# Performance work log

Measured on AMD Instinct MI355X. Metric: run time of the kernel, lower is better.

## Reference

```python
import jax, jax.numpy as jnp
import numpy as np

INPUT_DIM = 32
HIDDEN = 64
BATCH = 4096
SEQ = 256


def _uniform(key, shape, bound):
    return jax.random.uniform(key, shape, dtype=jnp.float32, minval=-bound, maxval=bound)


def setup_inputs() -> dict:
    key = jax.random.key(0)
    ks = jax.random.split(key, 16)
    kb = 1.0 / np.sqrt(HIDDEN)  # torch LSTM/Linear init bound
    x = jax.random.normal(ks[0], (BATCH, SEQ, INPUT_DIM), dtype=jnp.float32)
    # LSTM layer 0 (input_dim -> hidden), gate order i,f,g,o stacked on dim 0
    Wih0 = _uniform(ks[1], (4 * HIDDEN, INPUT_DIM), kb)
    Whh0 = _uniform(ks[2], (4 * HIDDEN, HIDDEN), kb)
    bih0 = _uniform(ks[3], (4 * HIDDEN,), kb)
    bhh0 = _uniform(ks[4], (4 * HIDDEN,), kb)
    # LSTM layer 1 (hidden -> hidden)
    Wih1 = _uniform(ks[5], (4 * HIDDEN, HIDDEN), kb)
    Whh1 = _uniform(ks[6], (4 * HIDDEN, HIDDEN), kb)
    bih1 = _uniform(ks[7], (4 * HIDDEN,), kb)
    bhh1 = _uniform(ks[8], (4 * HIDDEN,), kb)
    # MLP head
    W1 = _uniform(ks[9], (HIDDEN, HIDDEN), kb)
    b1 = _uniform(ks[10], (HIDDEN,), kb)
    W2 = _uniform(ks[11], (1, HIDDEN), kb)
    b2 = _uniform(ks[12], (1,), kb)
    return {"x": x, "Wih0": Wih0, "Whh0": Whh0, "bih0": bih0, "bhh0": bhh0,
            "Wih1": Wih1, "Whh1": Whh1, "bih1": bih1, "bhh1": bhh1,
            "W1": W1, "b1": b1, "W2": W2, "b2": b2}


def lstm_layer(x, Wih, Whh, bih, bhh):
    """x: [B,T,D] -> hidden sequence [B,T,H]. PyTorch gate order i,f,g,o."""
    B = x.shape[0]
    H = Whh.shape[1]
    # precompute input contribution for all timesteps: [B,T,4H]
    gx = jnp.einsum('btd,gd->btg', x, Wih) + bih + bhh

    def step(carry, g_t):
        h, c = carry
        g = g_t + h @ Whh.T  # [B,4H]
        i, f, gg, o = jnp.split(g, 4, axis=-1)
        i = jax.nn.sigmoid(i)
        f = jax.nn.sigmoid(f)
        gg = jnp.tanh(gg)
        o = jax.nn.sigmoid(o)
        c = f * c + i * gg
        h = o * jnp.tanh(c)
        return (h, c), h

    h0 = jnp.zeros((B, H), x.dtype)
    c0 = jnp.zeros((B, H), x.dtype)
    _, hs = jax.lax.scan(step, (h0, c0), jnp.swapaxes(gx, 0, 1))  # hs: [T,B,H]
    return jnp.swapaxes(hs, 0, 1)


def reference(x, Wih0, Whh0, bih0, bhh0, Wih1, Whh1, bih1, bhh1, W1, b1, W2, b2):
    h1 = lstm_layer(x, Wih0, Whh0, bih0, bhh0)    # [B,T,H]
    h2 = lstm_layer(h1, Wih1, Whh1, bih1, bhh1)   # [B,T,H]
    last = h2[:, -1, :]                            # [B,H]
    f = jax.nn.relu(last @ W1.T + b1)              # dropout = identity (eval)
    out = f @ W2.T + b2                            # [B,1]
    return out
```

## Files before the change

### kernel.cpp

```cpp
#include <hip/hip_runtime.h>
#include <cstdint>

typedef __attribute__((ext_vector_type(8))) _Float16 f16x8;
typedef __attribute__((ext_vector_type(4))) float f32x4;

#define SEQL 256

#define WS_B0H   0
#define WS_B0L   49152
#define WS_B1H   98304
#define WS_BIAS0 229376
#define WS_BIAS1 230400

#define ASTR 528
#define L_HD 8448
#define HDSTR 272
#define LDS_TOTAL 12800

#define NEG_L   -1.4426950408889634f
#define NEG_2L  -2.8853900817779268f
#define LO_SCALE 2048.0f
#define LO_INV   4.8828125e-4f

__device__ __forceinline__ float ex2(float x) { return __builtin_amdgcn_exp2f(x); }
__device__ __forceinline__ float rcp_(float x) { return __builtin_amdgcn_rcpf(x); }
__device__ __forceinline__ f32x4 mfma16(f16x8 a, f16x8 b, f32x4 c) {
  return __builtin_amdgcn_mfma_f32_16x16x32_f16(a, b, c, 0, 0, 0);
}
__device__ __forceinline__ f16x8 zero8() {
  f16x8 z;
#pragma unroll
  for (int i = 0; i < 8; ++i) z[i] = (_Float16)0.f;
  return z;
}
__device__ __forceinline__ f16x8 cvt8(f32x4 a, f32x4 b) {
  f16x8 r;
#pragma unroll
  for (int j = 0; j < 4; ++j) r[j] = (_Float16)a[j];
#pragma unroll
  for (int j = 0; j < 4; ++j) r[4 + j] = (_Float16)b[j];
  return r;
}
__device__ __forceinline__ unsigned f16bits(float h) {
  _Float16 hf = (_Float16)h;
  unsigned short us;
  __builtin_memcpy(&us, &hf, 2);
  return (unsigned)us;
}

__device__ __forceinline__ int cp(int p) {
  return (p & ~3) | ((p & 1) << 1) | ((p >> 1) & 1);
}

__global__ __launch_bounds__(256) void prep(
    const float* __restrict__ Wih0, const float* __restrict__ Whh0,
    const float* __restrict__ bih0, const float* __restrict__ bhh0,
    const float* __restrict__ Wih1, const float* __restrict__ Whh1,
    const float* __restrict__ bih1, const float* __restrict__ bhh1,
    unsigned char* __restrict__ ws) {
  int e = blockIdx.x * 256 + threadIdx.x;
  if (e < 24576) {
    int j = e & 7, lane = (e >> 3) & 63, nt = (e >> 9) & 15, ks = e >> 13;
    int kdim = ks * 32 + (lane >> 4) * 8 + j;
    int col = nt * 16 + (lane & 15);
    int ko = col >> 2, g = col & 3;
    float w = (kdim < 32) ? Wih0[(g * 64 + ko) * 32 + kdim]
                          : Whh0[(g * 64 + ko) * 64 + cp(kdim - 32)];
    w *= (g == 2) ? NEG_2L : NEG_L;
    _Float16 hi = (_Float16)w;
    _Float16 lo = (_Float16)((w - (float)hi) * LO_SCALE);
    ((_Float16*)(ws + WS_B0H))[e] = hi;
    ((_Float16*)(ws + WS_B0L))[e] = lo;
  } else if (e < 57344) {
    int r = e - 24576;
    int j = r & 7, lane = (r >> 3) & 63, nt = (r >> 9) & 15, ks = r >> 13;
    int kdim = ks * 32 + (lane >> 4) * 8 + j;
    int col = nt * 16 + (lane & 15);
    int ko = col >> 2, g = col & 3;
    float w = (kdim < 64) ? Wih1[(g * 64 + ko) * 64 + cp(kdim)]
                          : Whh1[(g * 64 + ko) * 64 + cp(kdim - 64)];
    w *= (g == 2) ? NEG_2L : NEG_L;
    _Float16 hi = (_Float16)w;
    _Float16 lo = (_Float16)((w - (float)hi) * LO_SCALE);
    ((_Float16*)(ws + WS_B1H))[r] = hi;
    ((_Float16*)(ws + WS_B1H + 65536))[r] = lo;
  } else if (e < 57856) {
    int r = e - 57344;
    int col = r & 255, ko = col >> 2, g = col & 3;
    float v = (r < 256) ? bih0[g * 64 + ko] + bhh0[g * 64 + ko]
                        : bih1[g * 64 + ko] + bhh1[g * 64 + ko];
    v *= (g == 2) ? NEG_2L : NEG_L;
    ((float*)(ws + (r < 256 ? WS_BIAS0 : WS_BIAS1)))[col] = v;
  }
}

__global__ __launch_bounds__(1024, 4) void lstm_mfma12(
    const float* __restrict__ x, const unsigned char* __restrict__ ws,
    const float* __restrict__ W1, const float* __restrict__ b1,
    const float* __restrict__ W2, const float* __restrict__ b2,
    float* __restrict__ out) {
  __shared__ __align__(16) unsigned char lds[LDS_TOTAL];
  const int tid = threadIdx.x;
  const int lane = tid & 63, wave = tid >> 6;
  const int q = lane >> 4, mcol = lane & 15;

  f16x8 b0h[3], b0l[3], b1h[4], b1l[4];
#pragma unroll
  for (int ks = 0; ks < 3; ++ks) {
    int rec = (ks * 16 + wave) * 64 + lane;
    b0h[ks] = ((const f16x8*)(ws + WS_B0H))[rec];
    b0l[ks] = ((const f16x8*)(ws + WS_B0L))[rec];
  }
#pragma unroll
  for (int ks = 0; ks < 4; ++ks) {
    int rec = (ks * 16 + wave) * 64 + lane;
    b1h[ks] = ((const f16x8*)(ws + WS_B1H))[rec];
    b1l[ks] = ((const f16x8*)(ws + WS_B1H + 65536))[rec];
  }
  const f32x4 bias0v = ((const f32x4*)(ws + WS_BIAS0))[wave * 4 + q];
  const f32x4 bias1v = ((const f32x4*)(ws + WS_BIAS1))[wave * 4 + q];
  f32x4 z4;
  z4[0] = z4[1] = z4[2] = z4[3] = 0.f;

  for (int i = tid; i < 2112; i += 1024) ((unsigned*)lds)[i] = 0u;

  const float* xp = x + (size_t)(blockIdx.x * 16 + mcol) * (SEQL * 32) + q * 8;
  f16x8 ax = cvt8(*(const f32x4*)(xp), *(const f32x4*)(xp + 4));
  f32x4 xa = *(const f32x4*)(xp + 32);

  const int ard = mcol * ASTR + q * 16;

  float c1 = 0.f, c2 = 0.f, h2f = 0.f;
  f16x8 ah1[2], ah2[2];
  ah1[0] = ah1[1] = ah2[0] = ah2[1] = zero8();
  __syncthreads();

  auto cell = [&](const f32x4& aH, const f32x4& aL, float& c) -> float {
    float p0 = fmaf(aL[0], LO_INV, aH[0]);
    float p1 = fmaf(aL[1], LO_INV, aH[1]);
    float p2 = fmaf(aL[2], LO_INV, aH[2]);
    float p3 = fmaf(aL[3], LO_INV, aH[3]);
    float A = ex2(p0), F = ex2(p1), B = ex2(p2), C = ex2(p3);
    float ig = (1.f - B) * rcp_((1.f + A) * (1.f + B));
    float gf = rcp_(1.f + F);
    c = fmaf(gf, c, ig);
    float D = ex2(fminf(c * NEG_2L, 100.f));
    return (1.f - D) * rcp_((1.f + C) * (1.f + D));
  };

  auto hwrite = [&](float h, int slot) {
    int hb = (int)f16bits(h);
    int partner = __shfl_xor(hb, 32, 64);
    if (lane < 32) {
      unsigned v = ((unsigned)hb & 0xffffu) | ((unsigned)partner << 16);
      *(unsigned*)(lds + mcol * ASTR + slot + wave * 8 + q * 4) = v;
    }
  };

  auto iter = [&](int t, int par, bool doL2) {
    const int h1s = par * 128;
    const int h2s = 256 + par * 128;
    const int tn1 = (t + 1 < SEQL) ? t + 1 : SEQL - 1;
    const int tn2 = (t + 2 < SEQL) ? t + 2 : SEQL - 1;
    f32x4 xb = *(const f32x4*)(xp + tn1 * 32 + 4);

    f32x4 aH0, aL0, aH1, aL1;
    aH0 = mfma16(b0h[0], ax, bias0v);
    aL0 = mfma16(b0l[0], ax, z4);
    aH1 = mfma16(b1h[0], ah1[0], bias1v);
    aL1 = mfma16(b1l[0], ah1[0], z4);
    aH0 = mfma16(b0h[1], ah1[0], aH0);
    aL0 = mfma16(b0l[1], ah1[0], aL0);
    aH1 = mfma16(b1h[1], ah1[1], aH1);
    aL1 = mfma16(b1l[1], ah1[1], aL1);
    aH0 = mfma16(b0h[2], ah1[1], aH0);
    aL0 = mfma16(b0l[2], ah1[1], aL0);
    aH1 = mfma16(b1h[2], ah2[0], aH1);
    aL1 = mfma16(b1l[2], ah2[0], aL1);
    aH1 = mfma16(b1h[3], ah2[1], aH1);
    aL1 = mfma16(b1l[3], ah2[1], aL1);

    float h1 = cell(aH0, aL0, c1);
    hwrite(h1, h1s);
    if (doL2) {
      float h2 = cell(aH1, aL1, c2);
      hwrite(h2, h2s);
    }
    ax = cvt8(xa, xb);
    xa = *(const f32x4*)(xp + tn2 * 32);
    __syncthreads();
    ah1[0] = *(const f16x8*)(lds + ard + h1s);
    ah1[1] = *(const f16x8*)(lds + ard + h1s + 64);
    ah2[0] = *(const f16x8*)(lds + ard + h2s);
    ah2[1] = *(const f16x8*)(lds + ard + h2s + 64);
  };

  iter(0, 0, false);
#pragma unroll 1
  for (int tp = 0; tp < 127; ++tp) {
    iter(2 * tp + 1, 1, true);
    iter(2 * tp + 2, 0, true);
  }
  iter(255, 1, true);

  {
    f32x4 aH = mfma16(b1h[0], ah1[0], bias1v);
    f32x4 aL = mfma16(b1l[0], ah1[0], z4);
    aH = mfma16(b1h[1], ah1[1], aH);
    aL = mfma16(b1l[1], ah1[1], aL);
#pragma unroll
    for (int ks = 0; ks < 2; ++ks) {
      aH = mfma16(b1h[ks + 2], ah2[ks], aH);
      aL = mfma16(b1l[ks + 2], ah2[ks], aL);
    }
    h2f = cell(aH, aL, c2);
  }

  __syncthreads();
  *(float*)(lds + L_HD + mcol * HDSTR + (wave * 4 + q) * 4) = h2f;
  __syncthreads();
  if (tid < 256) {
    const int s = tid & 15, bo = tid >> 4;
    const float* h2row = (const float*)(lds + L_HD + bo * HDSTR);
    float partial = 0.f;
#pragma unroll
    for (int kk4 = 0; kk4 < 4; ++kk4) {
      int kk = s * 4 + kk4;
      float f = b1[kk];
#pragma unroll
      for (int j = 0; j < 64; j += 4) {
        f32x4 w = *(const f32x4*)(W1 + kk * 64 + j);
        f = fmaf(w[0], h2row[j], f);
        f = fmaf(w[1], h2row[j + 1], f);
        f = fmaf(w[2], h2row[j + 2], f);
        f = fmaf(w[3], h2row[j + 3], f);
      }
      f = fmaxf(f, 0.f);
      partial = fmaf(f, W2[kk], partial);
    }
    partial += __shfl_xor(partial, 8, 64);
    partial += __shfl_xor(partial, 4, 64);
    partial += __shfl_xor(partial, 2, 64);
    partial += __shfl_xor(partial, 1, 64);
    if (s == 0) out[blockIdx.x * 16 + bo] = partial + b2[0];
  }
}

extern "C" void kernel_launch(void* const* d_in, const int* in_sizes, int n_in,
                              void* d_out, int out_size, void* d_ws, size_t ws_size,
                              hipStream_t stream) {
  const float* x    = (const float*)d_in[0];
  const float* Wih0 = (const float*)d_in[1];
  const float* Whh0 = (const float*)d_in[2];
  const float* bih0 = (const float*)d_in[3];
  const float* bhh0 = (const float*)d_in[4];
  const float* Wih1 = (const float*)d_in[5];
  const float* Whh1 = (const float*)d_in[6];
  const float* bih1 = (const float*)d_in[7];
  const float* bhh1 = (const float*)d_in[8];
  const float* W1   = (const float*)d_in[9];
  const float* b1   = (const float*)d_in[10];
  const float* W2   = (const float*)d_in[11];
  const float* b2   = (const float*)d_in[12];
  unsigned char* ws = (unsigned char*)d_ws;
  float* out = (float*)d_out;

  prep<<<(57856 + 255) / 256, 256, 0, stream>>>(Wih0, Whh0, bih0, bhh0,
                                                Wih1, Whh1, bih1, bhh1, ws);
  lstm_mfma12<<<256, 1024, 0, stream>>>(x, ws, W1, b1, W2, b2, out);
}
```

Baseline: 455.6 us.

## Restructure LSTM kernel to 4-wave blocks of 8 sequences with FP8 low-part correction

Shrinks each block from 16 waves and 16 sequences to 4 waves and 8 sequences, launching twice as many blocks. Each wave now computes four gate column tiles and keeps the fp16 high weights in registers. The low-order weight correction moves from fp16 MFMA to fp8 MFMA, with low weights staged in LDS and hidden states stored in both fp16 and fp8. The aim is a cheaper per-step barrier and more blocks in flight, at the cost of half the MFMA rows being idle, more LDS traffic, and less accurate fp8 low parts.

```diff
diff --git a/kernel.cpp b/kernel.cpp
--- a/kernel.cpp
+++ b/kernel.cpp
@@ -3,19 +3,24 @@
 
 typedef __attribute__((ext_vector_type(8))) _Float16 f16x8;
 typedef __attribute__((ext_vector_type(4))) float f32x4;
+typedef __attribute__((ext_vector_type(4))) int i32x4;
 
 #define SEQL 256
 
 #define WS_B0H   0
-#define WS_B0L   49152
-#define WS_B1H   98304
-#define WS_BIAS0 229376
-#define WS_BIAS1 230400
-
-#define ASTR 528
-#define L_HD 8448
-#define HDSTR 272
-#define LDS_TOTAL 12800
+#define WS_B1H   49152
+#define WS_LO8   114688
+#define WS_BIAS  172032
+
+#define L_LO8   0
+#define L_FEX   57344
+#define FEXSTR  528
+#define L_8EX   65792
+#define EX8STR  272
+#define L_BIAS  70144
+#define L_HD    72192
+#define HDSTR   272
+#define LDS_TOTAL 74368
 
 #define NEG_L   -1.4426950408889634f
 #define NEG_2L  -2.8853900817779268f
@@ -27,6 +32,9 @@
 __device__ __forceinline__ f32x4 mfma16(f16x8 a, f16x8 b, f32x4 c) {
   return __builtin_amdgcn_mfma_f32_16x16x32_f16(a, b, c, 0, 0, 0);
 }
+__device__ __forceinline__ f32x4 mfma8(long a, long b, f32x4 c) {
+  return __builtin_amdgcn_mfma_f32_16x16x32_fp8_fp8(a, b, c, 0, 0, 0);
+}
 __device__ __forceinline__ f16x8 zero8() {
   f16x8 z;
 #pragma unroll
@@ -41,15 +49,15 @@
   for (int j = 0; j < 4; ++j) r[4 + j] = (_Float16)b[j];
   return r;
 }
-__device__ __forceinline__ unsigned f16bits(float h) {
-  _Float16 hf = (_Float16)h;
-  unsigned short us;
-  __builtin_memcpy(&us, &hf, 2);
-  return (unsigned)us;
-}
-
-__device__ __forceinline__ int cp(int p) {
-  return (p & ~3) | ((p & 1) << 1) | ((p >> 1) & 1);
+__device__ __forceinline__ long packfp8(f32x4 a, f32x4 b) {
+  int lo = __builtin_amdgcn_cvt_pk_fp8_f32(a[0], a[1], 0, false);
+  lo = __builtin_amdgcn_cvt_pk_fp8_f32(a[2], a[3], lo, true);
+  int hi = __builtin_amdgcn_cvt_pk_fp8_f32(b[0], b[1], 0, false);
+  hi = __builtin_amdgcn_cvt_pk_fp8_f32(b[2], b[3], hi, true);
+  return ((long)(unsigned)hi << 32) | (unsigned)lo;
+}
+__device__ __forceinline__ unsigned char fp8byte(float v) {
+  return (unsigned char)(__builtin_amdgcn_cvt_pk_fp8_f32(v, v, 0, false) & 0xff);
 }
 
 __global__ __launch_bounds__(256) void prep(
@@ -65,36 +73,36 @@
     int col = nt * 16 + (lane & 15);
     int ko = col >> 2, g = col & 3;
     float w = (kdim < 32) ? Wih0[(g * 64 + ko) * 32 + kdim]
-                          : Whh0[(g * 64 + ko) * 64 + cp(kdim - 32)];
+                          : Whh0[(g * 64 + ko) * 64 + (kdim - 32)];
     w *= (g == 2) ? NEG_2L : NEG_L;
     _Float16 hi = (_Float16)w;
-    _Float16 lo = (_Float16)((w - (float)hi) * LO_SCALE);
+    float lo = (w - (float)hi) * LO_SCALE;
     ((_Float16*)(ws + WS_B0H))[e] = hi;
-    ((_Float16*)(ws + WS_B0L))[e] = lo;
+    (ws + WS_LO8)[e] = fp8byte(lo);
   } else if (e < 57344) {
     int r = e - 24576;
     int j = r & 7, lane = (r >> 3) & 63, nt = (r >> 9) & 15, ks = r >> 13;
     int kdim = ks * 32 + (lane >> 4) * 8 + j;
     int col = nt * 16 + (lane & 15);
     int ko = col >> 2, g = col & 3;
-    float w = (kdim < 64) ? Wih1[(g * 64 + ko) * 64 + cp(kdim)]
-                          : Whh1[(g * 64 + ko) * 64 + cp(kdim - 64)];
+    float w = (kdim < 64) ? Wih1[(g * 64 + ko) * 64 + kdim]
+                          : Whh1[(g * 64 + ko) * 64 + (kdim - 64)];
     w *= (g == 2) ? NEG_2L : NEG_L;
     _Float16 hi = (_Float16)w;
-    _Float16 lo = (_Float16)((w - (float)hi) * LO_SCALE);
+    float lo = (w - (float)hi) * LO_SCALE;
     ((_Float16*)(ws + WS_B1H))[r] = hi;
-    ((_Float16*)(ws + WS_B1H + 65536))[r] = lo;
+    (ws + WS_LO8 + 24576)[r] = fp8byte(lo);
   } else if (e < 57856) {
     int r = e - 57344;
     int col = r & 255, ko = col >> 2, g = col & 3;
     float v = (r < 256) ? bih0[g * 64 + ko] + bhh0[g * 64 + ko]
                         : bih1[g * 64 + ko] + bhh1[g * 64 + ko];
     v *= (g == 2) ? NEG_2L : NEG_L;
-    ((float*)(ws + (r < 256 ? WS_BIAS0 : WS_BIAS1)))[col] = v;
-  }
-}
-
-__global__ __launch_bounds__(1024, 4) void lstm_mfma12(
+    ((float*)(ws + WS_BIAS))[r] = v;
+  }
+}
+
+__global__ __launch_bounds__(256, 2) void lstm_mfma13(
     const float* __restrict__ x, const unsigned char* __restrict__ ws,
     const float* __restrict__ W1, const float* __restrict__ b1,
     const float* __restrict__ W2, const float* __restrict__ b2,
@@ -103,96 +111,140 @@
   const int tid = threadIdx.x;
   const int lane = tid & 63, wave = tid >> 6;
   const int q = lane >> 4, mcol = lane & 15;
-
-  f16x8 b0h[3], b0l[3], b1h[4], b1l[4];
-#pragma unroll
-  for (int ks = 0; ks < 3; ++ks) {
-    int rec = (ks * 16 + wave) * 64 + lane;
-    b0h[ks] = ((const f16x8*)(ws + WS_B0H))[rec];
-    b0l[ks] = ((const f16x8*)(ws + WS_B0L))[rec];
-  }
-#pragma unroll
-  for (int ks = 0; ks < 4; ++ks) {
-    int rec = (ks * 16 + wave) * 64 + lane;
-    b1h[ks] = ((const f16x8*)(ws + WS_B1H))[rec];
-    b1l[ks] = ((const f16x8*)(ws + WS_B1H + 65536))[rec];
-  }
-  const f32x4 bias0v = ((const f32x4*)(ws + WS_BIAS0))[wave * 4 + q];
-  const f32x4 bias1v = ((const f32x4*)(ws + WS_BIAS1))[wave * 4 + q];
+  const bool act = mcol < 8;
+
+  for (int i = tid; i < 3584; i += 256)
+    ((i32x4*)(lds + L_LO8))[i] = ((const i32x4*)(ws + WS_LO8))[i];
+  for (int i = tid; i < 512; i += 256)
+    ((float*)(lds + L_BIAS))[i] = ((const float*)(ws + WS_BIAS))[i];
+  for (int i = tid; i < 3200; i += 256)
+    ((unsigned*)(lds + L_FEX))[i] = 0u;
+
+  f16x8 w0h[4][3], w1h[4][4];
+#pragma unroll
+  for (int m = 0; m < 4; ++m) {
+    const int nt = wave + 4 * m;
+#pragma unroll
+    for (int ks = 0; ks < 3; ++ks)
+      w0h[m][ks] = ((const f16x8*)(ws + WS_B0H))[(ks * 16 + nt) * 64 + lane];
+#pragma unroll
+    for (int ks = 0; ks < 4; ++ks)
+      w1h[m][ks] = ((const f16x8*)(ws + WS_B1H))[(ks * 16 + nt) * 64 + lane];
+  }
   f32x4 z4;
   z4[0] = z4[1] = z4[2] = z4[3] = 0.f;
 
-  for (int i = tid; i < 2112; i += 1024) ((unsigned*)lds)[i] = 0u;
-
-  const float* xp = x + (size_t)(blockIdx.x * 16 + mcol) * (SEQL * 32) + q * 8;
-  f16x8 ax = cvt8(*(const f32x4*)(xp), *(const f32x4*)(xp + 4));
-  f32x4 xa = *(const f32x4*)(xp + 32);
-
-  const int ard = mcol * ASTR + q * 16;
-
-  float c1 = 0.f, c2 = 0.f, h2f = 0.f;
-  f16x8 ah1[2], ah2[2];
-  ah1[0] = ah1[1] = ah2[0] = ah2[1] = zero8();
+  const float* xp =
+      x + (size_t)(blockIdx.x * 8 + (mcol & 7)) * (SEQL * 32) + q * 8;
+  f32x4 xa = *(const f32x4*)(xp);
+  f32x4 xb = *(const f32x4*)(xp + 4);
+
   __syncthreads();
 
-  auto cell = [&](const f32x4& aH, const f32x4& aL, float& c) -> float {
-    float p0 = fmaf(aL[0], LO_INV, aH[0]);
-    float p1 = fmaf(aL[1], LO_INV, aH[1]);
-    float p2 = fmaf(aL[2], LO_INV, aH[2]);
-    float p3 = fmaf(aL[3], LO_INV, aH[3]);
+  f16x8 ax = cvt8(xa, xb);
+  long ax8 = packfp8(xa, xb);
+  f16x8 ah1f[2], ah2f[2];
+  ah1f[0] = ah1f[1] = ah2f[0] = ah2f[1] = zero8();
+  long fh1[2] = {0, 0}, fh2[2] = {0, 0};
+  float c1[4] = {0.f, 0.f, 0.f, 0.f}, c2[4] = {0.f, 0.f, 0.f, 0.f};
+
+  const int rdF = mcol * FEXSTR + q * 16;
+  const int rd8 = mcol * EX8STR + q * 8;
+
+  auto lo0 = [&](int ks, int m) -> long {
+    return *(const long*)(lds + L_LO8 + ((ks * 16 + wave + 4 * m) * 64 + lane) * 8);
+  };
+  auto lo1 = [&](int ks, int m) -> long {
+    return *(const long*)(lds + L_LO8 + 24576 +
+                          ((ks * 16 + wave + 4 * m) * 64 + lane) * 8);
+  };
+
+  auto cellfn = [&](const f32x4& aH, const f32x4& aL, const f32x4& bv,
+                    float& c) -> float {
+    float p0 = fmaf(aL[0], LO_INV, aH[0]) + bv[0];
+    float p1 = fmaf(aL[1], LO_INV, aH[1]) + bv[1];
+    float p2 = fmaf(aL[2], LO_INV, aH[2]) + bv[2];
+    float p3 = fmaf(aL[3], LO_INV, aH[3]) + bv[3];
     float A = ex2(p0), F = ex2(p1), B = ex2(p2), C = ex2(p3);
     float ig = (1.f - B) * rcp_((1.f + A) * (1.f + B));
-    float gf = rcp_(1.f + F);
-    c = fmaf(gf, c, ig);
+    c = fmaf(rcp_(1.f + F), c, ig);
     float D = ex2(fminf(c * NEG_2L, 100.f));
     return (1.f - D) * rcp_((1.f + C) * (1.f + D));
   };
 
-  auto hwrite = [&](float h, int slot) {
-    int hb = (int)f16bits(h);
-    int partner = __shfl_xor(hb, 32, 64);
-    if (lane < 32) {
-      unsigned v = ((unsigned)hb & 0xffffu) | ((unsigned)partner << 16);
-      *(unsigned*)(lds + mcol * ASTR + slot + wave * 8 + q * 4) = v;
-    }
-  };
-
   auto iter = [&](int t, int par, bool doL2) {
-    const int h1s = par * 128;
-    const int h2s = 256 + par * 128;
-    const int tn1 = (t + 1 < SEQL) ? t + 1 : SEQL - 1;
-    const int tn2 = (t + 2 < SEQL) ? t + 2 : SEQL - 1;
-    f32x4 xb = *(const f32x4*)(xp + tn1 * 32 + 4);
-
-    f32x4 aH0, aL0, aH1, aL1;
-    aH0 = mfma16(b0h[0], ax, bias0v);
-    aL0 = mfma16(b0l[0], ax, z4);
-    aH1 = mfma16(b1h[0], ah1[0], bias1v);
-    aL1 = mfma16(b1l[0], ah1[0], z4);
-    aH0 = mfma16(b0h[1], ah1[0], aH0);
-    aL0 = mfma16(b0l[1], ah1[0], aL0);
-    aH1 = mfma16(b1h[1], ah1[1], aH1);
-    aL1 = mfma16(b1l[1], ah1[1], aL1);
-    aH0 = mfma16(b0h[2], ah1[1], aH0);
-    aL0 = mfma16(b0l[2], ah1[1], aL0);
-    aH1 = mfma16(b1h[2], ah2[0], aH1);
-    aL1 = mfma16(b1l[2], ah2[0], aL1);
-    aH1 = mfma16(b1h[3], ah2[1], aH1);
-    aL1 = mfma16(b1l[3], ah2[1], aL1);
-
-    float h1 = cell(aH0, aL0, c1);
-    hwrite(h1, h1s);
+    const int h1sF = par * 128, h2sF = 256 + par * 128;
+    const int h1s8 = par * 64, h2s8 = 128 + par * 64;
+    int tn = (t + 1 < SEQL) ? t + 1 : SEQL - 1;
+    xa = *(const f32x4*)(xp + tn * 32);
+    xb = *(const f32x4*)(xp + tn * 32 + 4);
+
+    f32x4 aH[4], aL[4];
+#pragma unroll
+    for (int m = 0; m < 4; ++m) aH[m] = mfma16(w0h[m][0], ax, z4);
+#pragma unroll
+    for (int m = 0; m < 4; ++m) aL[m] = mfma8(lo0(0, m), ax8, z4);
+#pragma unroll
+    for (int ks = 0; ks < 2; ++ks) {
+#pragma unroll
+      for (int m = 0; m < 4; ++m)
+        aH[m] = mfma16(w0h[m][ks + 1], ah1f[ks], aH[m]);
+#pragma unroll
+      for (int m = 0; m < 4; ++m)
+        aL[m] = mfma8(lo0(ks + 1, m), fh1[ks], aL[m]);
+    }
+#pragma unroll
+    for (int m = 0; m < 4; ++m) {
+      const int cell = 4 * wave + 16 * m + q;
+      f32x4 bv = *(const f32x4*)(lds + L_BIAS + cell * 16);
+      float h = cellfn(aH[m], aL[m], bv, c1[m]);
+      if (act) {
+        *(_Float16*)(lds + L_FEX + mcol * FEXSTR + h1sF + cell * 2) =
+            (_Float16)h;
+        (lds + L_8EX + mcol * EX8STR + h1s8)[cell] = fp8byte(h);
+      }
+    }
+#pragma unroll
+    for (int m = 0; m < 4; ++m) aH[m] = mfma16(w1h[m][0], ah1f[0], z4);
+#pragma unroll
+    for (int m = 0; m < 4; ++m) aL[m] = mfma8(lo1(0, m), fh1[0], z4);
+#pragma unroll
+    for (int m = 0; m < 4; ++m) aH[m] = mfma16(w1h[m][1], ah1f[1], aH[m]);
+#pragma unroll
+    for (int m = 0; m < 4; ++m) aL[m] = mfma8(lo1(1, m), fh1[1], aL[m]);
+#pragma unroll
+    for (int ks = 0; ks < 2; ++ks) {
+#pragma unroll
+      for (int m = 0; m < 4; ++m)
+        aH[m] = mfma16(w1h[m][ks + 2], ah2f[ks], aH[m]);
+#pragma unroll
+      for (int m = 0; m < 4; ++m)
+        aL[m] = mfma8(lo1(ks + 2, m), fh2[ks], aL[m]);
+    }
     if (doL2) {
-      float h2 = cell(aH1, aL1, c2);
-      hwrite(h2, h2s);
-    }
+#pragma unroll
+      for (int m = 0; m < 4; ++m) {
+        const int cell = 4 * wave + 16 * m + q;
+        f32x4 bv = *(const f32x4*)(lds + L_BIAS + 1024 + cell * 16);
+        float h = cellfn(aH[m], aL[m], bv, c2[m]);
+        if (act) {
+          *(_Float16*)(lds + L_FEX + mcol * FEXSTR + h2sF + cell * 2) =
+              (_Float16)h;
+          (lds + L_8EX + mcol * EX8STR + h2s8)[cell] = fp8byte(h);
+        }
+      }
+    }
+    __syncthreads();
+    ah1f[0] = *(const f16x8*)(lds + L_FEX + rdF + h1sF);
+    ah1f[1] = *(const f16x8*)(lds + L_FEX + rdF + h1sF + 64);
+    ah2f[0] = *(const f16x8*)(lds + L_FEX + rdF + h2sF);
+    ah2f[1] = *(const f16x8*)(lds + L_FEX + rdF + h2sF + 64);
+    fh1[0] = *(const long*)(lds + L_8EX + rd8 + h1s8);
+    fh1[1] = *(const long*)(lds + L_8EX + rd8 + h1s8 + 32);
+    fh2[0] = *(const long*)(lds + L_8EX + rd8 + h2s8);
+    fh2[1] = *(const long*)(lds + L_8EX + rd8 + h2s8 + 32);
     ax = cvt8(xa, xb);
-    xa = *(const f32x4*)(xp + tn2 * 32);
-    __syncthreads();
-    ah1[0] = *(const f16x8*)(lds + ard + h1s);
-    ah1[1] = *(const f16x8*)(lds + ard + h1s + 64);
-    ah2[0] = *(const f16x8*)(lds + ard + h2s);
-    ah2[1] = *(const f16x8*)(lds + ard + h2s + 64);
+    ax8 = packfp8(xa, xb);
   };
 
   iter(0, 0, false);
@@ -204,22 +256,35 @@
   iter(255, 1, true);
 
   {
-    f32x4 aH = mfma16(b1h[0], ah1[0], bias1v);
-    f32x4 aL = mfma16(b1l[0], ah1[0], z4);
-    aH = mfma16(b1h[1], ah1[1], aH);
-    aL = mfma16(b1l[1], ah1[1], aL);
+    f32x4 aH[4], aL[4];
+#pragma unroll
+    for (int m = 0; m < 4; ++m) aH[m] = mfma16(w1h[m][0], ah1f[0], z4);
+#pragma unroll
+    for (int m = 0; m < 4; ++m) aL[m] = mfma8(lo1(0, m), fh1[0], z4);
+#pragma unroll
+    for (int m = 0; m < 4; ++m) aH[m] = mfma16(w1h[m][1], ah1f[1], aH[m]);
+#pragma unroll
+    for (int m = 0; m < 4; ++m) aL[m] = mfma8(lo1(1, m), fh1[1], aL[m]);
 #pragma unroll
     for (int ks = 0; ks < 2; ++ks) {
-      aH = mfma16(b1h[ks + 2], ah2[ks], aH);
-      aL = mfma16(b1l[ks + 2], ah2[ks], aL);
-    }
-    h2f = cell(aH, aL, c2);
-  }
-
+#pragma unroll
+      for (int m = 0; m < 4; ++m)
+        aH[m] = mfma16(w1h[m][ks + 2], ah2f[ks], aH[m]);
+#pragma unroll
+      for (int m = 0; m < 4; ++m)
+        aL[m] = mfma8(lo1(ks + 2, m), fh2[ks], aL[m]);
+    }
+#pragma unroll
+    for (int m = 0; m < 4; ++m) {
+      const int cell = 4 * wave + 16 * m + q;
+      f32x4 bv = *(const f32x4*)(lds + L_BIAS + 1024 + cell * 16);
+      float h = cellfn(aH[m], aL[m], bv, c2[m]);
+      if (act) *(float*)(lds + L_HD + mcol * HDSTR + cell * 4) = h;
+    }
+  }
   __syncthreads();
-  *(float*)(lds + L_HD + mcol * HDSTR + (wave * 4 + q) * 4) = h2f;
-  __syncthreads();
-  if (tid < 256) {
+
+  if (tid < 128) {
     const int s = tid & 15, bo = tid >> 4;
     const float* h2row = (const float*)(lds + L_HD + bo * HDSTR);
     float partial = 0.f;
@@ -242,7 +307,7 @@
     partial += __shfl_xor(partial, 4, 64);
     partial += __shfl_xor(partial, 2, 64);
     partial += __shfl_xor(partial, 1, 64);
-    if (s == 0) out[blockIdx.x * 16 + bo] = partial + b2[0];
+    if (s == 0) out[blockIdx.x * 8 + bo] = partial + b2[0];
   }
 }
 
@@ -267,5 +332,5 @@
 
   prep<<<(57856 + 255) / 256, 256, 0, stream>>>(Wih0, Whh0, bih0, bhh0,
                                                 Wih1, Whh1, bih1, bhh1, ws);
-  lstm_mfma12<<<256, 1024, 0, stream>>>(x, ws, W1, b1, W2, b2, out);
-}
+  lstm_mfma13<<<512, 256, 0, stream>>>(x, ws, W1, b1, W2, b2, out);
+}
```

Result: slower. 714.3 us (+56.8%).

## Write h directly as f16 to LDS, drop shuffle and permutation, reorder MFMAs

Applied to the files above, without the earlier changes.

Each lane now stores its hidden value as a single f16 into LDS at a natural position. This removes the cross-lane shuffle and packed 32-bit write, and drops the cp() k-permutation from the weight prep. The layer-0 MFMAs and cell now run first, followed by a sched_barrier and then the layer-1 MFMAs, so layer-1 matrix work can overlap layer-0 transcendental math. The x prefetch is also simplified to load both halves two steps ahead. The cost is twice as many narrow 16-bit LDS stores and the possibility of bank conflicts.

```diff
diff --git a/kernel.cpp b/kernel.cpp
--- a/kernel.cpp
+++ b/kernel.cpp
@@ -40,16 +40,6 @@
 #pragma unroll
   for (int j = 0; j < 4; ++j) r[4 + j] = (_Float16)b[j];
   return r;
-}
-__device__ __forceinline__ unsigned f16bits(float h) {
-  _Float16 hf = (_Float16)h;
-  unsigned short us;
-  __builtin_memcpy(&us, &hf, 2);
-  return (unsigned)us;
-}
-
-__device__ __forceinline__ int cp(int p) {
-  return (p & ~3) | ((p & 1) << 1) | ((p >> 1) & 1);
 }
 
 __global__ __launch_bounds__(256) void prep(
@@ -65,7 +55,7 @@
     int col = nt * 16 + (lane & 15);
     int ko = col >> 2, g = col & 3;
     float w = (kdim < 32) ? Wih0[(g * 64 + ko) * 32 + kdim]
-                          : Whh0[(g * 64 + ko) * 64 + cp(kdim - 32)];
+                          : Whh0[(g * 64 + ko) * 64 + (kdim - 32)];
     w *= (g == 2) ? NEG_2L : NEG_L;
     _Float16 hi = (_Float16)w;
     _Float16 lo = (_Float16)((w - (float)hi) * LO_SCALE);
@@ -77,8 +67,8 @@
     int kdim = ks * 32 + (lane >> 4) * 8 + j;
     int col = nt * 16 + (lane & 15);
     int ko = col >> 2, g = col & 3;
-    float w = (kdim < 64) ? Wih1[(g * 64 + ko) * 64 + cp(kdim)]
-                          : Whh1[(g * 64 + ko) * 64 + cp(kdim - 64)];
+    float w = (kdim < 64) ? Wih1[(g * 64 + ko) * 64 + kdim]
+                          : Whh1[(g * 64 + ko) * 64 + (kdim - 64)];
     w *= (g == 2) ? NEG_2L : NEG_L;
     _Float16 hi = (_Float16)w;
     _Float16 lo = (_Float16)((w - (float)hi) * LO_SCALE);
@@ -94,7 +84,7 @@
   }
 }
 
-__global__ __launch_bounds__(1024, 4) void lstm_mfma12(
+__global__ __launch_bounds__(1024, 4) void lstm_mfma14(
     const float* __restrict__ x, const unsigned char* __restrict__ ws,
     const float* __restrict__ W1, const float* __restrict__ b1,
     const float* __restrict__ W2, const float* __restrict__ b2,
@@ -127,8 +117,10 @@
   const float* xp = x + (size_t)(blockIdx.x * 16 + mcol) * (SEQL * 32) + q * 8;
   f16x8 ax = cvt8(*(const f32x4*)(xp), *(const f32x4*)(xp + 4));
   f32x4 xa = *(const f32x4*)(xp + 32);
+  f32x4 xb = *(const f32x4*)(xp + 36);
 
   const int ard = mcol * ASTR + q * 16;
+  const int hwr = mcol * ASTR + (wave * 4 + q) * 2;
 
   float c1 = 0.f, c2 = 0.f, h2f = 0.f;
   f16x8 ah1[2], ah2[2];
@@ -142,52 +134,40 @@
     float p3 = fmaf(aL[3], LO_INV, aH[3]);
     float A = ex2(p0), F = ex2(p1), B = ex2(p2), C = ex2(p3);
     float ig = (1.f - B) * rcp_((1.f + A) * (1.f + B));
-    float gf = rcp_(1.f + F);
-    c = fmaf(gf, c, ig);
+    c = fmaf(rcp_(1.f + F), c, ig);
     float D = ex2(fminf(c * NEG_2L, 100.f));
     return (1.f - D) * rcp_((1.f + C) * (1.f + D));
   };
 
-  auto hwrite = [&](float h, int slot) {
-    int hb = (int)f16bits(h);
-    int partner = __shfl_xor(hb, 32, 64);
-    if (lane < 32) {
-      unsigned v = ((unsigned)hb & 0xffffu) | ((unsigned)partner << 16);
-      *(unsigned*)(lds + mcol * ASTR + slot + wave * 8 + q * 4) = v;
-    }
-  };
-
   auto iter = [&](int t, int par, bool doL2) {
     const int h1s = par * 128;
     const int h2s = 256 + par * 128;
-    const int tn1 = (t + 1 < SEQL) ? t + 1 : SEQL - 1;
-    const int tn2 = (t + 2 < SEQL) ? t + 2 : SEQL - 1;
-    f32x4 xb = *(const f32x4*)(xp + tn1 * 32 + 4);
-
-    f32x4 aH0, aL0, aH1, aL1;
-    aH0 = mfma16(b0h[0], ax, bias0v);
-    aL0 = mfma16(b0l[0], ax, z4);
-    aH1 = mfma16(b1h[0], ah1[0], bias1v);
-    aL1 = mfma16(b1l[0], ah1[0], z4);
+
+    f32x4 aH0 = mfma16(b0h[0], ax, bias0v);
+    f32x4 aL0 = mfma16(b0l[0], ax, z4);
     aH0 = mfma16(b0h[1], ah1[0], aH0);
     aL0 = mfma16(b0l[1], ah1[0], aL0);
+    aH0 = mfma16(b0h[2], ah1[1], aH0);
+    aL0 = mfma16(b0l[2], ah1[1], aL0);
+    float h1 = cell(aH0, aL0, c1);
+    *(_Float16*)(lds + hwr + h1s) = (_Float16)h1;
+    __builtin_amdgcn_sched_barrier(0);
+    f32x4 aH1 = mfma16(b1h[0], ah1[0], bias1v);
+    f32x4 aL1 = mfma16(b1l[0], ah1[0], z4);
     aH1 = mfma16(b1h[1], ah1[1], aH1);
     aL1 = mfma16(b1l[1], ah1[1], aL1);
-    aH0 = mfma16(b0h[2], ah1[1], aH0);
-    aL0 = mfma16(b0l[2], ah1[1], aL0);
     aH1 = mfma16(b1h[2], ah2[0], aH1);
     aL1 = mfma16(b1l[2], ah2[0], aL1);
     aH1 = mfma16(b1h[3], ah2[1], aH1);
     aL1 = mfma16(b1l[3], ah2[1], aL1);
-
-    float h1 = cell(aH0, aL0, c1);
-    hwrite(h1, h1s);
     if (doL2) {
       float h2 = cell(aH1, aL1, c2);
-      hwrite(h2, h2s);
+      *(_Float16*)(lds + hwr + h2s) = (_Float16)h2;
     }
     ax = cvt8(xa, xb);
-    xa = *(const f32x4*)(xp + tn2 * 32);
+    int tn = t + 2; if (tn > SEQL - 1) tn = SEQL - 1;
+    xa = *(const f32x4*)(xp + tn * 32);
+    xb = *(const f32x4*)(xp + tn * 32 + 4);
     __syncthreads();
     ah1[0] = *(const f16x8*)(lds + ard + h1s);
     ah1[1] = *(const f16x8*)(lds + ard + h1s + 64);
@@ -267,5 +247,5 @@
 
   prep<<<(57856 + 255) / 256, 256, 0, stream>>>(Wih0, Whh0, bih0, bhh0,
                                                 Wih1, Whh1, bih1, bhh1, ws);
-  lstm_mfma12<<<256, 1024, 0, stream>>>(x, ws, W1, b1, W2, b2, out);
-}
+  lstm_mfma14<<<256, 1024, 0, stream>>>(x, ws, W1, b1, W2, b2, out);
+}
```

New measurement: 452.7 us. About the same (-0.6%).
